# Kernel tuning notes

Measured on AMD Instinct MI355X. Metric: run time of the kernel, lower is better.

The kernel has to match this reference:

```python
import jax, jax.numpy as jnp
import numpy as np

BS, LX, LY, D, H, DK = 2, 2048, 2048, 1024, 16, 64


def setup_inputs() -> dict:
    key = jax.random.key(0)
    ks = jax.random.split(key, 12)
    s = 1.0 / np.sqrt(D)
    return {
        "x": jax.random.normal(ks[0], (BS, LX, D), jnp.float32),
        "y": jax.random.normal(ks[1], (BS, LY, D), jnp.float32),
        "mask": jnp.zeros((BS, 1, LX, LY), jnp.float32),
        "Wq": jax.random.normal(ks[2], (D, H * DK), jnp.float32) * s,
        "bq": jnp.zeros((H * DK,), jnp.float32),
        "Wk": jax.random.normal(ks[3], (D, H * DK), jnp.float32) * s,
        "bk": jnp.zeros((H * DK,), jnp.float32),
        "Wv": jax.random.normal(ks[4], (D, H * DK), jnp.float32) * s,
        "bv": jnp.zeros((H * DK,), jnp.float32),
        "Wo": jax.random.normal(ks[5], (H * DK, D), jnp.float32) * s,
        "bo": jnp.zeros((D,), jnp.float32),
    }


def reference(x, y, mask, Wq, bq, Wk, bk, Wv, bv, Wo, bo):
    bs, lx, _ = x.shape
    ly = y.shape[1]
    norm = DK ** 0.5
    # projections -> (bs, len, H, DK)
    q = (x @ Wq + bq).reshape(bs, lx, H, DK)
    k = (y @ Wk + bk).reshape(bs, ly, H, DK)
    v = (y @ Wv + bv).reshape(bs, ly, H, DK)
    # scores: (bs, H, lx, ly)
    scores = jnp.einsum('bxhd,byhd->bhxy', q, k) / norm + mask
    attn = jax.nn.softmax(scores, axis=-1)
    # output: (bs, lx, H, DK) -> (bs, lx, H*DK)
    out = jnp.einsum('bhxy,byhd->bxhd', attn, v).reshape(bs, lx, H * DK)
    return out @ Wo + bo
```

## Files before the change

### kernel.cpp

```cpp
#include <hip/hip_runtime.h>
#include <hip/hip_bf16.h>


typedef __bf16 bf16;
typedef __bf16 bf16x2 __attribute__((ext_vector_type(2)));
typedef __bf16 bf16x4 __attribute__((ext_vector_type(4)));
typedef __bf16 bf16x8 __attribute__((ext_vector_type(8)));
typedef float floatx4 __attribute__((ext_vector_type(4)));
typedef unsigned int uintx4 __attribute__((ext_vector_type(4)));

#define MFMA16(a, b, c) __builtin_amdgcn_mfma_f32_16x16x32_bf16(a, b, c, 0, 0, 0)

constexpr int BS = 2, LX = 2048, LY = 2048, D = 1024, H = 16, DK = 64;
constexpr int HD = H * DK;
constexpr float LOG2E = 1.4426950408889634f;

__device__ __forceinline__ void cp16(const bf16* g, bf16* l) {
  __builtin_amdgcn_global_load_lds(
      (const __attribute__((address_space(1))) unsigned int*)g,
      (__attribute__((address_space(3))) unsigned int*)l, 16, 0, 0);
}

__device__ __forceinline__ unsigned pk2(float a, float b) {
  bf16x2 p;
  p[0] = (bf16)a;
  p[1] = (bf16)b;
  return __builtin_bit_cast(unsigned, p);
}

__global__ __launch_bounds__(256) void prep(const float* __restrict__ W0, bf16* __restrict__ T0,
                                            const float* __restrict__ W1, bf16* __restrict__ T1,
                                            const float* __restrict__ W2, bf16* __restrict__ T2,
                                            const float* __restrict__ W3, bf16* __restrict__ T3,
                                            const float* __restrict__ x, bf16* __restrict__ xb,
                                            const float* __restrict__ y, bf16* __restrict__ yb,
                                            const float* __restrict__ mask, int* __restrict__ flags) {
  const int id = blockIdx.x;
  const int t = threadIdx.x;
  if (id < 1024) {
    __shared__ bf16 tile[64][72];
    const float* W;
    bf16* T;
    switch (id >> 8) {
      case 0: W = W0; T = T0; break;
      case 1: W = W1; T = T1; break;
      case 2: W = W2; T = T2; break;
      default: W = W3; T = T3; break;
    }
    const int kt = id & 15, nt = (id >> 4) & 15;
    const int r = t >> 2, c4 = (t & 3) * 16;
    const float* src = W + (size_t)(kt * 64 + r) * 1024 + nt * 64 + c4;
#pragma unroll
    for (int i = 0; i < 16; i++) tile[r][c4 + i] = (bf16)src[i];
    __syncthreads();
    bf16 vals[16];
#pragma unroll
    for (int i = 0; i < 16; i++) vals[i] = tile[c4 + i][r];
    bf16* dst = T + (size_t)(nt * 64 + r) * 1024 + kt * 64 + c4;
#pragma unroll
    for (int i = 0; i < 16; i++) dst[i] = vals[i];
  } else if (id < 5120) {
    const int id2 = id - 1024;
    const float* src = (id2 >= 2048) ? y : x;
    bf16* dst = (id2 >= 2048) ? yb : xb;
    const size_t i = ((size_t)(id2 & 2047) * 256 + t) * 8;
    float4 a = *(const float4*)(src + i);
    float4 c = *(const float4*)(src + i + 4);
    bf16 tmp[8] = {(bf16)a.x, (bf16)a.y, (bf16)a.z, (bf16)a.w,
                   (bf16)c.x, (bf16)c.y, (bf16)c.z, (bf16)c.w};
    *(bf16x8*)(dst + i) = *(const bf16x8*)tmp;
  } else {
    const int id3 = id - 5120;
    const int region = id3 >> 5, sub = id3 & 31;
    const float4* p = (const float4*)mask + (size_t)region * 65536 + sub * 2048;
    bool nz = false;
#pragma unroll
    for (int it = 0; it < 8; it++) {
      float4 v = p[it * 256 + t];
      nz |= (v.x != 0.f) | (v.y != 0.f) | (v.z != 0.f) | (v.w != 0.f);
    }
    if (nz) atomicOr(&flags[region], 1);
  }
}

__global__ __launch_bounds__(512, 2) void qkv8(const bf16* __restrict__ xb, const bf16* __restrict__ yb,
                                               const bf16* __restrict__ Wtq, const bf16* __restrict__ Wtk,
                                               const bf16* __restrict__ Wtv,
                                               const float* __restrict__ bq, const float* __restrict__ bk,
                                               const float* __restrict__ bv,
                                               bf16* __restrict__ Qb, bf16* __restrict__ Kb,
                                               bf16* __restrict__ Vt) {
  constexpr int K = 1024, N = 1024;
  __shared__ __align__(16) bf16 As[2][2][128 * 64];
  __shared__ __align__(16) bf16 Bs[2][2][128 * 64];

  const int z = blockIdx.z;
  const bf16* A = (z == 0) ? xb : yb;
  const bf16* Bt = (z == 0) ? Wtq : (z == 1) ? Wtk : Wtv;
  const float* bias = (z == 0) ? bq : (z == 1) ? bk : bv;

  const int t = threadIdx.x;
  const int w = t >> 6, lane = t & 63, quad = lane >> 4, l15 = lane & 15;
  const int wm = w >> 2, wn = w & 3;
  const int mbase = blockIdx.y * 256, nbase = blockIdx.x * 256;
  const int srow = lane >> 3, schunk = (lane & 7) ^ srow;
  const int sx = quad ^ (l15 & 7);

  floatx4 acc[2][4][2][2] = {};
  bf16x8 af[4][2];
  bf16x8 bfr[2][2][2];

#define ST_A(ktt, half, slot)                                                                 \
  {                                                                                           \
    _Pragma("unroll") for (int j = 0; j < 2; j++) {                                           \
      const int r0 = w * 16 + j * 8;                                                          \
      cp16(A + (size_t)(mbase + (half) * 128 + r0 + srow) * K + (ktt) * 64 + schunk * 8,      \
           &As[slot][half][r0 * 64]);                                                         \
    }                                                                                         \
  }
#define ST_B(ktt, half, slot)                                                                 \
  {                                                                                           \
    _Pragma("unroll") for (int j = 0; j < 2; j++) {                                           \
      const int r0 = w * 16 + j * 8;                                                          \
      cp16(Bt + (size_t)(nbase + (half) * 128 + r0 + srow) * K + (ktt) * 64 + schunk * 8,     \
           &Bs[slot][half][r0 * 64]);                                                         \
    }                                                                                         \
  }
#define LOAD_A(slot, mh)                                                                      \
  {                                                                                           \
    _Pragma("unroll") for (int i = 0; i < 4; i++) {                                           \
      const bf16* p = &As[slot][mh][(wm * 64 + i * 16 + l15) * 64];                           \
      af[i][0] = *(const bf16x8*)(p + sx * 8);                                                \
      af[i][1] = *(const bf16x8*)(p + (sx ^ 4) * 8);                                          \
    }                                                                                         \
  }
#define LOAD_B(slot, nh)                                                                      \
  {                                                                                           \
    _Pragma("unroll") for (int j = 0; j < 2; j++) {                                           \
      const bf16* p = &Bs[slot][nh][(wn * 32 + j * 16 + l15) * 64];                           \
      bfr[nh][j][0] = *(const bf16x8*)(p + sx * 8);                                           \
      bfr[nh][j][1] = *(const bf16x8*)(p + (sx ^ 4) * 8);                                     \
    }                                                                                         \
  }
#define MFMA_Q(mh, nh)                                                                        \
  {                                                                                           \
    _Pragma("unroll") for (int i = 0; i < 4; i++)                                             \
        _Pragma("unroll") for (int j = 0; j < 2; j++) {                                       \
      acc[mh][i][nh][j] = MFMA16(af[i][0], bfr[nh][j][0], acc[mh][i][nh][j]);                 \
      acc[mh][i][nh][j] = MFMA16(af[i][1], bfr[nh][j][1], acc[mh][i][nh][j]);                 \
    }                                                                                         \
  }
#define BARX()                       \
  {                                  \
    asm volatile("" ::: "memory");   \
    __builtin_amdgcn_s_barrier();    \
    asm volatile("" ::: "memory");   \
  }
#define VMW(n) asm volatile("s_waitcnt vmcnt(" #n ")" ::: "memory")
#define LG0() asm volatile("s_waitcnt lgkmcnt(0)" ::: "memory")
#define NOPST {}
#define TILE_BODY(PAR, STG0, V0, STG1, V1, STG2, STG3, V3)  \
  {                                                         \
    LOAD_A(PAR, 0);                                         \
    LOAD_B(PAR, 0);                                         \
    STG0;                                                   \
    V0;                                                     \
    BARX();                                                 \
    LG0();                                                  \
    __builtin_amdgcn_s_setprio(1);                          \
    MFMA_Q(0, 0);                                           \
    __builtin_amdgcn_s_setprio(0);                          \
    BARX();                                                 \
    LOAD_B(PAR, 1);                                         \
    STG1;                                                   \
    V1;                                                     \
    BARX();                                                 \
    LG0();                                                  \
    __builtin_amdgcn_s_setprio(1);                          \
    MFMA_Q(0, 1);                                           \
    __builtin_amdgcn_s_setprio(0);                          \
    BARX();                                                 \
    LOAD_A(PAR, 1);                                         \
    STG2;                                                   \
    BARX();                                                 \
    LG0();                                                  \
    __builtin_amdgcn_s_setprio(1);                          \
    MFMA_Q(1, 0);                                           \
    __builtin_amdgcn_s_setprio(0);                          \
    BARX();                                                 \
    STG3;                                                   \
    V3;                                                     \
    BARX();                                                 \
    LG0();                                                  \
    __builtin_amdgcn_s_setprio(1);                          \
    MFMA_Q(1, 1);                                           \
    __builtin_amdgcn_s_setprio(0);                          \
    BARX();                                                 \
  }

  ST_A(0, 0, 0);
  ST_B(0, 0, 0);
  ST_B(0, 1, 0);
  ST_A(0, 1, 0);
  ST_A(1, 0, 1);
  ST_B(1, 0, 1);
  VMW(8);
  BARX();

#pragma unroll 1
  for (int kt = 0; kt < 14; kt += 2) {
    TILE_BODY(0, ST_B(kt + 1, 1, 1), VMW(8), ST_A(kt + 1, 1, 1), VMW(8),
              ST_A(kt + 2, 0, 0), ST_B(kt + 2, 0, 0), VMW(8));
    TILE_BODY(1, ST_B(kt + 2, 1, 0), VMW(8), ST_A(kt + 2, 1, 0), VMW(8),
              ST_A(kt + 3, 0, 1), ST_B(kt + 3, 0, 1), VMW(8));
  }
  TILE_BODY(0, ST_B(15, 1, 1), VMW(8), ST_A(15, 1, 1), VMW(8), NOPST, NOPST, VMW(4));
  TILE_BODY(1, NOPST, VMW(2), NOPST, VMW(0), NOPST, NOPST, NOPST);

#undef TILE_BODY
#undef NOPST
#undef LG0
#undef VMW
#undef BARX
#undef MFMA_Q
#undef LOAD_B
#undef LOAD_A
#undef ST_B
#undef ST_A

  if (z <= 1) {
    bf16* outp = (z == 0) ? Qb : Kb;
    const float sc = (z == 0) ? 0.125f * LOG2E : 1.0f;
#pragma unroll
    for (int nh = 0; nh < 2; nh++)
#pragma unroll
      for (int j = 0; j < 2; j++) {
        const int n = nbase + nh * 128 + wn * 32 + j * 16 + l15;
        const float bv2 = bias[n];
#pragma unroll
        for (int mh = 0; mh < 2; mh++)
#pragma unroll
          for (int i = 0; i < 4; i++)
#pragma unroll
            for (int r = 0; r < 4; r++) {
              const int m = mbase + mh * 128 + wm * 64 + i * 16 + quad * 4 + r;
              outp[(size_t)m * N + n] = (bf16)((acc[mh][i][nh][j][r] + bv2) * sc);
            }
      }
  } else {
    const int b = mbase >> 11;
    const int y0 = mbase & 2047;
#pragma unroll
    for (int nh = 0; nh < 2; nh++)
#pragma unroll
      for (int j = 0; j < 2; j++) {
        const int n = nbase + nh * 128 + wn * 32 + j * 16 + l15;
        const float bv2 = bias[n];
        const int hh = n >> 6, dk = n & 63;
        bf16* dst0 = Vt + ((size_t)(b * H + hh) * DK + dk) * LY + y0;
#pragma unroll
        for (int mh = 0; mh < 2; mh++)
#pragma unroll
          for (int i = 0; i < 4; i++) {
            const int yy = mh * 128 + wm * 64 + i * 16 + quad * 4;
            bf16 tmp[4];
#pragma unroll
            for (int r = 0; r < 4; r++) tmp[r] = (bf16)(acc[mh][i][nh][j][r] + bv2);
            *(bf16x4*)(dst0 + yy) = *(const bf16x4*)tmp;
          }
      }
  }
}

__global__ __launch_bounds__(256) void out_gemm(const bf16* __restrict__ A, const bf16* __restrict__ Bt,
                                                const float* __restrict__ bias, float* __restrict__ outp) {
  constexpr int K = 1024, N = 1024;
  __shared__ __align__(16) bf16 As[128 * 64];
  __shared__ __align__(16) bf16 Bs[64 * 64];
  const int t = threadIdx.x;
  const int w = t >> 6, lane = t & 63, quad = lane >> 4, l15 = lane & 15;
  const int mbase = blockIdx.y * 128, nbase = blockIdx.x * 64;
  const int srow = lane >> 3, schunk = (lane & 7) ^ srow;
  const int sx = quad ^ (l15 & 7);

  floatx4 acc[2][4] = {};
  for (int k0 = 0; k0 < K; k0 += 64) {
    __syncthreads();
#pragma unroll
    for (int j = 0; j < 4; j++) {
      const int r0 = w * 32 + j * 8;
      cp16(A + (size_t)(mbase + r0 + srow) * K + k0 + schunk * 8, As + r0 * 64);
    }
#pragma unroll
    for (int j = 0; j < 2; j++) {
      const int r0 = w * 16 + j * 8;
      cp16(Bt + (size_t)(nbase + r0 + srow) * K + k0 + schunk * 8, Bs + r0 * 64);
    }
    __syncthreads();
    bf16x8 af[2][2], bfr[4][2];
#pragma unroll
    for (int i = 0; i < 2; i++) {
      const int ra = w * 32 + i * 16 + l15;
      af[i][0] = *(const bf16x8*)&As[ra * 64 + sx * 8];
      af[i][1] = *(const bf16x8*)&As[ra * 64 + (sx ^ 4) * 8];
    }
#pragma unroll
    for (int jn = 0; jn < 4; jn++) {
      const int rb = jn * 16 + l15;
      bfr[jn][0] = *(const bf16x8*)&Bs[rb * 64 + sx * 8];
      bfr[jn][1] = *(const bf16x8*)&Bs[rb * 64 + (sx ^ 4) * 8];
    }
#pragma unroll
    for (int i = 0; i < 2; i++)
#pragma unroll
      for (int jn = 0; jn < 4; jn++) {
        acc[i][jn] = MFMA16(af[i][0], bfr[jn][0], acc[i][jn]);
        acc[i][jn] = MFMA16(af[i][1], bfr[jn][1], acc[i][jn]);
      }
  }
#pragma unroll
  for (int jn = 0; jn < 4; jn++) {
    const int n = nbase + jn * 16 + l15;
    const float bv2 = bias[n];
#pragma unroll
    for (int i = 0; i < 2; i++)
#pragma unroll
      for (int r = 0; r < 4; r++) {
        const int m = mbase + w * 32 + i * 16 + quad * 4 + r;
        outp[(size_t)m * N + n] = acc[i][jn][r] + bv2;
      }
  }
}

__global__ __launch_bounds__(256, 2) void attn9(const bf16* __restrict__ Q, const bf16* __restrict__ Kb,
                                                const bf16* __restrict__ Vt, const float* __restrict__ mask,
                                                const int* __restrict__ flags, bf16* __restrict__ Hout) {
  __shared__ __align__(16) bf16 Ks[2][64 * 64];
  __shared__ __align__(16) bf16 Vs[2][64 * 64];
  const int t = threadIdx.x;
  const int w = t >> 6, lane = t & 63, quad = lane >> 4, l15 = lane & 15;
  const int xt = blockIdx.x, h = blockIdx.y, b = blockIdx.z;
  const int qbase = xt * 128 + w * 32;
  const int srow = lane >> 3, schunk = (lane & 7) ^ srow;
  const int sx = quad ^ (l15 & 7);

  bf16x8 qf[2][2];
#pragma unroll
  for (int rt = 0; rt < 2; rt++) {
    const bf16* qrow = Q + (size_t)(b * LX + qbase + rt * 16 + l15) * HD + h * DK;
    qf[rt][0] = *(const bf16x8*)(qrow + quad * 8);
    qf[rt][1] = *(const bf16x8*)(qrow + 32 + quad * 8);
  }
  const int mflag = flags[b * 16 + xt];

  bf16 onearr[8];
#pragma unroll
  for (int i = 0; i < 8; i++) onearr[i] = (bf16)((l15 == 0) ? 1.0f : 0.0f);
  const bf16x8 onesf = *(const bf16x8*)onearr;

  floatx4 o[2][4] = {};
  floatx4 ol[2] = {};

  const bf16* Kbase = Kb + (size_t)b * LY * HD + h * DK;
  const bf16* Vbase = Vt + (size_t)(b * H + h) * DK * LY;
  const float* mbase2 = mask + (size_t)(b * LX + qbase + l15) * LY;

#define STAGE(yt, bufi)                                                               \
  {                                                                                   \
    _Pragma("unroll") for (int j = 0; j < 2; j++) {                                   \
      const int r0 = w * 16 + j * 8;                                                  \
      cp16(Kbase + (size_t)((yt) + r0 + srow) * HD + schunk * 8, &Ks[bufi][r0 * 64]); \
      cp16(Vbase + (size_t)(r0 + srow) * LY + (yt) + schunk * 8, &Vs[bufi][r0 * 64]); \
    }                                                                                 \
  }

#define TILE(yt, BUF)                                                                       \
  {                                                                                         \
    const bf16* KsB = Ks[BUF];                                                              \
    const bf16* VsB = Vs[BUF];                                                              \
    bf16x8 kf[4][2];                                                                        \
    _Pragma("unroll") for (int nt = 0; nt < 4; nt++) {                                      \
      const int ry = nt * 16 + l15;                                                         \
      kf[nt][0] = *(const bf16x8*)&KsB[ry * 64 + sx * 8];                                   \
      kf[nt][1] = *(const bf16x8*)&KsB[ry * 64 + (sx ^ 4) * 8];                             \
    }                                                                                       \
    floatx4 s[2][4] = {};                                                                   \
    __builtin_amdgcn_s_setprio(1);                                                          \
    _Pragma("unroll") for (int nt = 0; nt < 4; nt++)                                        \
        _Pragma("unroll") for (int rt = 0; rt < 2; rt++) {                                  \
      s[rt][nt] = MFMA16(kf[nt][0], qf[rt][0], s[rt][nt]);                                  \
      s[rt][nt] = MFMA16(kf[nt][1], qf[rt][1], s[rt][nt]);                                  \
    }                                                                                       \
    __builtin_amdgcn_s_setprio(0);                                                          \
    if (mflag) {                                                                            \
      _Pragma("unroll") for (int rt = 0; rt < 2; rt++)                                      \
          _Pragma("unroll") for (int nt = 0; nt < 4; nt++) {                                \
        const float* mp = mbase2 + (size_t)rt * 16 * LY + (yt) + nt * 16 + quad * 4;        \
        float4 mv = *(const float4*)mp;                                                     \
        s[rt][nt][0] = fminf(s[rt][nt][0] + LOG2E * mv.x, 30.f);                            \
        s[rt][nt][1] = fminf(s[rt][nt][1] + LOG2E * mv.y, 30.f);                            \
        s[rt][nt][2] = fminf(s[rt][nt][2] + LOG2E * mv.z, 30.f);                            \
        s[rt][nt][3] = fminf(s[rt][nt][3] + LOG2E * mv.w, 30.f);                            \
      }                                                                                     \
    }                                                                                       \
    bf16x8 pf[2][2];                                                                        \
    _Pragma("unroll") for (int rt = 0; rt < 2; rt++) {                                      \
      uintx4 wd0, wd1;                                                                      \
      _Pragma("unroll") for (int F = 0; F < 2; F++)                                         \
          _Pragma("unroll") for (int hh = 0; hh < 2; hh++) {                                \
        unsigned wa = pk2(__builtin_amdgcn_exp2f(s[rt][2 * F][2 * hh]),                     \
                          __builtin_amdgcn_exp2f(s[rt][2 * F][2 * hh + 1]));                \
        unsigned wb = pk2(__builtin_amdgcn_exp2f(s[rt][2 * F + 1][2 * hh]),                 \
                          __builtin_amdgcn_exp2f(s[rt][2 * F + 1][2 * hh + 1]));            \
        asm("v_permlane32_swap_b32 %0, %1" : "+v"(wa), "+v"(wb));                           \
        asm("v_permlane16_swap_b32 %0, %1" : "+v"(wa), "+v"(wb));                           \
        if (F == 0) {                                                                       \
          wd0[hh] = wa;                                                                     \
          wd0[hh + 2] = wb;                                                                 \
        } else {                                                                            \
          wd1[hh] = wa;                                                                     \
          wd1[hh + 2] = wb;                                                                 \
        }                                                                                   \
      }                                                                                     \
      pf[rt][0] = __builtin_bit_cast(bf16x8, wd0);                                          \
      pf[rt][1] = __builtin_bit_cast(bf16x8, wd1);                                          \
    }                                                                                       \
    __builtin_amdgcn_s_setprio(1);                                                          \
    _Pragma("unroll") for (int u = 0; u < 4; u++) {                                         \
      const int rd = u * 16 + l15;                                                          \
      bf16x8 v0 = *(const bf16x8*)&VsB[rd * 64 + sx * 8];                                   \
      bf16x8 v1 = *(const bf16x8*)&VsB[rd * 64 + (sx ^ 4) * 8];                             \
      _Pragma("unroll") for (int rt = 0; rt < 2; rt++) {                                    \
        o[rt][u] = MFMA16(pf[rt][0], v0, o[rt][u]);                                         \
        o[rt][u] = MFMA16(pf[rt][1], v1, o[rt][u]);                                         \
      }                                                                                     \
    }                                                                                       \
    _Pragma("unroll") for (int rt = 0; rt < 2; rt++) {                                      \
      ol[rt] = MFMA16(pf[rt][0], onesf, ol[rt]);                                            \
      ol[rt] = MFMA16(pf[rt][1], onesf, ol[rt]);                                            \
    }                                                                                       \
    __builtin_amdgcn_s_setprio(0);                                                          \
  }

  STAGE(0, 0);
  for (int yt = 0; yt < LY; yt += 128) {
    __syncthreads();
    STAGE(yt + 64, 1);
    TILE(yt, 0);
    __syncthreads();
    if (yt + 128 < LY) STAGE(yt + 128, 0);
    TILE(yt + 64, 1);
  }

#pragma unroll
  for (int rt = 0; rt < 2; rt++)
#pragma unroll
    for (int r = 0; r < 4; r++) {
      const float lsum = __shfl(ol[rt][r], lane & 48, 64);
      const float rl = 1.0f / lsum;
      const int m = b * LX + qbase + rt * 16 + quad * 4 + r;
#pragma unroll
      for (int u = 0; u < 4; u++)
        Hout[(size_t)m * HD + h * DK + u * 16 + l15] = (bf16)(o[rt][u][r] * rl);
    }
#undef STAGE
#undef TILE
}

extern "C" void kernel_launch(void* const* d_in, const int* in_sizes, int n_in,
                              void* d_out, int out_size, void* d_ws, size_t ws_size,
                              hipStream_t stream) {
  const float* x = (const float*)d_in[0];
  const float* y = (const float*)d_in[1];
  const float* mask = (const float*)d_in[2];
  const float* Wq = (const float*)d_in[3];
  const float* bq = (const float*)d_in[4];
  const float* Wk = (const float*)d_in[5];
  const float* bk = (const float*)d_in[6];
  const float* Wv = (const float*)d_in[7];
  const float* bv = (const float*)d_in[8];
  const float* Wo = (const float*)d_in[9];
  const float* bo = (const float*)d_in[10];

  char* ws = (char*)d_ws;
  size_t off = 0;
  int* flags = (int*)(ws + off); off += 256;
  bf16* Qb = (bf16*)(ws + off); off += (size_t)BS * LX * HD * 2;
  bf16* Kb = (bf16*)(ws + off); off += (size_t)BS * LY * HD * 2;
  bf16* Vt = (bf16*)(ws + off); off += (size_t)BS * LY * HD * 2;
  bf16* Hb = (bf16*)(ws + off); off += (size_t)BS * LX * HD * 2;
  bf16* xbf = (bf16*)(ws + off); off += (size_t)BS * LX * D * 2;
  bf16* ybf = (bf16*)(ws + off); off += (size_t)BS * LY * D * 2;
  bf16* Wtq = (bf16*)(ws + off); off += (size_t)D * HD * 2;
  bf16* Wtk = (bf16*)(ws + off); off += (size_t)D * HD * 2;
  bf16* Wtv = (bf16*)(ws + off); off += (size_t)D * HD * 2;
  bf16* Wto = (bf16*)(ws + off); off += (size_t)HD * D * 2;

  dim3 blk(256);
  hipMemsetAsync(flags, 0, 32 * sizeof(int), stream);
  prep<<<dim3(6144), blk, 0, stream>>>(Wq, Wtq, Wk, Wtk, Wv, Wtv, Wo, Wto, x, xbf, y, ybf, mask, flags);
  qkv8<<<dim3(4, 16, 3), dim3(512), 0, stream>>>(xbf, ybf, Wtq, Wtk, Wtv, bq, bk, bv, Qb, Kb, Vt);
  attn9<<<dim3(16, 16, 2), blk, 0, stream>>>(Qb, Kb, Vt, mask, flags, Hb);
  out_gemm<<<dim3(16, 32), blk, 0, stream>>>(Hb, Wto, bo, (float*)d_out);
}
```

Measured before the change: 226.5 us.

## Load K/V fragments directly from global into registers, drop LDS staging

The attention kernel no longer stages K and V tiles in shared memory with async copies and barriers. Each wave loads its K and V MFMA fragments straight from global memory into registers, with K for the next tile prefetched during the current one. The grid is also flattened and remapped so that blocks sharing the same (batch, head) K/V data are grouped for L2 locality. This removes LDS traffic and __syncthreads, but each of the four waves now fetches the same K/V data separately, and the extra registers may hurt occupancy.

```diff
diff --git a/kernel.cpp b/kernel.cpp
--- a/kernel.cpp
+++ b/kernel.cpp
@@ -332,17 +332,16 @@
   }
 }
 
-__global__ __launch_bounds__(256, 2) void attn9(const bf16* __restrict__ Q, const bf16* __restrict__ Kb,
-                                                const bf16* __restrict__ Vt, const float* __restrict__ mask,
-                                                const int* __restrict__ flags, bf16* __restrict__ Hout) {
-  __shared__ __align__(16) bf16 Ks[2][64 * 64];
-  __shared__ __align__(16) bf16 Vs[2][64 * 64];
+__global__ __launch_bounds__(256, 2) void attn10(const bf16* __restrict__ Q, const bf16* __restrict__ Kb,
+                                                 const bf16* __restrict__ Vt, const float* __restrict__ mask,
+                                                 const int* __restrict__ flags, bf16* __restrict__ Hout) {
   const int t = threadIdx.x;
   const int w = t >> 6, lane = t & 63, quad = lane >> 4, l15 = lane & 15;
-  const int xt = blockIdx.x, h = blockIdx.y, b = blockIdx.z;
+  const int flat = blockIdx.x;
+  const int gg = (flat & 7) | (((flat >> 3) >> 4) << 3);
+  const int xt = (flat >> 3) & 15;
+  const int h = gg & 15, b = gg >> 4;
   const int qbase = xt * 128 + w * 32;
-  const int srow = lane >> 3, schunk = (lane & 7) ^ srow;
-  const int sx = quad ^ (l15 & 7);
 
   bf16x8 qf[2][2];
 #pragma unroll
@@ -361,35 +360,39 @@
   floatx4 o[2][4] = {};
   floatx4 ol[2] = {};
 
-  const bf16* Kbase = Kb + (size_t)b * LY * HD + h * DK;
-  const bf16* Vbase = Vt + (size_t)(b * H + h) * DK * LY;
+  const bf16* Kp = Kb + (size_t)(b * LY + l15) * HD + h * DK + quad * 8;
+  const bf16* Vp = Vt + ((size_t)(b * H + h) * DK + l15) * LY + quad * 8;
   const float* mbase2 = mask + (size_t)(b * LX + qbase + l15) * LY;
 
-#define STAGE(yt, bufi)                                                               \
-  {                                                                                   \
-    _Pragma("unroll") for (int j = 0; j < 2; j++) {                                   \
-      const int r0 = w * 16 + j * 8;                                                  \
-      cp16(Kbase + (size_t)((yt) + r0 + srow) * HD + schunk * 8, &Ks[bufi][r0 * 64]); \
-      cp16(Vbase + (size_t)(r0 + srow) * LY + (yt) + schunk * 8, &Vs[bufi][r0 * 64]); \
-    }                                                                                 \
-  }
-
-#define TILE(yt, BUF)                                                                       \
+  bf16x8 kfA[4][2], kfB[4][2], vf[4][2];
+
+#define LOADK(KF, yt)                                      \
+  {                                                        \
+    _Pragma("unroll") for (int nt = 0; nt < 4; nt++) {     \
+      const bf16* p = Kp + (size_t)((yt) + nt * 16) * HD;  \
+      KF[nt][0] = *(const bf16x8*)(p);                     \
+      KF[nt][1] = *(const bf16x8*)(p + 32);                \
+    }                                                      \
+  }
+#define LOADV(yt)                                          \
+  {                                                        \
+    _Pragma("unroll") for (int u = 0; u < 4; u++) {        \
+      const bf16* p = Vp + (size_t)(u * 16) * LY + (yt);   \
+      vf[u][0] = *(const bf16x8*)(p);                      \
+      vf[u][1] = *(const bf16x8*)(p + 32);                 \
+    }                                                      \
+  }
+
+#define TILE(KF, KFN, yt, PREF)                                                             \
   {                                                                                         \
-    const bf16* KsB = Ks[BUF];                                                              \
-    const bf16* VsB = Vs[BUF];                                                              \
-    bf16x8 kf[4][2];                                                                        \
-    _Pragma("unroll") for (int nt = 0; nt < 4; nt++) {                                      \
-      const int ry = nt * 16 + l15;                                                         \
-      kf[nt][0] = *(const bf16x8*)&KsB[ry * 64 + sx * 8];                                   \
-      kf[nt][1] = *(const bf16x8*)&KsB[ry * 64 + (sx ^ 4) * 8];                             \
-    }                                                                                       \
+    LOADV(yt);                                                                              \
+    if (PREF) LOADK(KFN, (yt) + 64);                                                        \
     floatx4 s[2][4] = {};                                                                   \
     __builtin_amdgcn_s_setprio(1);                                                          \
     _Pragma("unroll") for (int nt = 0; nt < 4; nt++)                                        \
         _Pragma("unroll") for (int rt = 0; rt < 2; rt++) {                                  \
-      s[rt][nt] = MFMA16(kf[nt][0], qf[rt][0], s[rt][nt]);                                  \
-      s[rt][nt] = MFMA16(kf[nt][1], qf[rt][1], s[rt][nt]);                                  \
+      s[rt][nt] = MFMA16(KF[nt][0], qf[rt][0], s[rt][nt]);                                  \
+      s[rt][nt] = MFMA16(KF[nt][1], qf[rt][1], s[rt][nt]);                                  \
     }                                                                                       \
     __builtin_amdgcn_s_setprio(0);                                                          \
     if (mflag) {                                                                            \
@@ -427,12 +430,9 @@
     }                                                                                       \
     __builtin_amdgcn_s_setprio(1);                                                          \
     _Pragma("unroll") for (int u = 0; u < 4; u++) {                                         \
-      const int rd = u * 16 + l15;                                                          \
-      bf16x8 v0 = *(const bf16x8*)&VsB[rd * 64 + sx * 8];                                   \
-      bf16x8 v1 = *(const bf16x8*)&VsB[rd * 64 + (sx ^ 4) * 8];                             \
       _Pragma("unroll") for (int rt = 0; rt < 2; rt++) {                                    \
-        o[rt][u] = MFMA16(pf[rt][0], v0, o[rt][u]);                                         \
-        o[rt][u] = MFMA16(pf[rt][1], v1, o[rt][u]);                                         \
+        o[rt][u] = MFMA16(pf[rt][0], vf[u][0], o[rt][u]);                                   \
+        o[rt][u] = MFMA16(pf[rt][1], vf[u][1], o[rt][u]);                                   \
       }                                                                                     \
     }                                                                                       \
     _Pragma("unroll") for (int rt = 0; rt < 2; rt++) {                                      \
@@ -442,14 +442,11 @@
     __builtin_amdgcn_s_setprio(0);                                                          \
   }
 
-  STAGE(0, 0);
+  LOADK(kfA, 0);
+#pragma unroll 1
   for (int yt = 0; yt < LY; yt += 128) {
-    __syncthreads();
-    STAGE(yt + 64, 1);
-    TILE(yt, 0);
-    __syncthreads();
-    if (yt + 128 < LY) STAGE(yt + 128, 0);
-    TILE(yt + 64, 1);
+    TILE(kfA, kfB, yt, true);
+    TILE(kfB, kfA, yt + 64, (yt + 128 < LY));
   }
 
 #pragma unroll
@@ -465,6 +462,8 @@
     }
 #undef STAGE
 #undef TILE
+#undef LOADK
+#undef LOADV
 }
 
 extern "C" void kernel_launch(void* const* d_in, const int* in_sizes, int n_in,
@@ -500,6 +499,6 @@
   hipMemsetAsync(flags, 0, 32 * sizeof(int), stream);
   prep<<<dim3(6144), blk, 0, stream>>>(Wq, Wtq, Wk, Wtk, Wv, Wtv, Wo, Wto, x, xbf, y, ybf, mask, flags);
   qkv8<<<dim3(4, 16, 3), dim3(512), 0, stream>>>(xbf, ybf, Wtq, Wtk, Wtv, bq, bk, bv, Qb, Kb, Vt);
-  attn9<<<dim3(16, 16, 2), blk, 0, stream>>>(Qb, Kb, Vt, mask, flags, Hb);
+  attn10<<<dim3(512), blk, 0, stream>>>(Qb, Kb, Vt, mask, flags, Hb);
   out_gemm<<<dim3(16, 32), blk, 0, stream>>>(Hb, Wto, bo, (float*)d_out);
 }
```

Result: slower. 299.2 us (+32.1%).
